# Kernel optimization log

Measured on AMD Instinct MI355X. Metric: run time of the kernel, lower is better.

Reference implementation:

```python
import jax, jax.numpy as jnp
import numpy as np

D_MODEL = 512
N_HEADS = 8
D_K = D_MODEL // N_HEADS  # 64
MAX_LEN = 5000


def _positional_encoding(d_model, max_len):
    pe = np.zeros((max_len, d_model), dtype=np.float32)
    position = np.arange(max_len, dtype=np.float32)[:, None]
    div_term = np.exp(np.arange(0, d_model, 2, dtype=np.float32) * (-np.log(10000.0) / d_model))
    pe[:, 0::2] = np.sin(position * div_term)
    pe[:, 1::2] = np.cos(position * div_term)
    return jnp.asarray(pe)


def _layer_norm(x, gamma, beta, eps):
    mu = jnp.mean(x, axis=-1, keepdims=True)
    var = jnp.mean(jnp.square(x - mu), axis=-1, keepdims=True)
    return (x - mu) * jax.lax.rsqrt(var + eps) * gamma + beta


def setup_inputs() -> dict:
    key = jax.random.key(0)
    ks = jax.random.split(key, 5)
    s = 1.0 / np.sqrt(D_MODEL)
    return {
        "x": jax.random.normal(ks[0], (4, 2048, D_MODEL), dtype=jnp.float32),
        "ln1_g": jnp.ones((D_MODEL,), jnp.float32),
        "ln1_b": jnp.zeros((D_MODEL,), jnp.float32),
        "wq": jax.random.normal(ks[1], (D_MODEL, D_MODEL), jnp.float32) * s,
        "wk": jax.random.normal(ks[2], (D_MODEL, D_MODEL), jnp.float32) * s,
        "wv": jax.random.normal(ks[3], (D_MODEL, D_MODEL), jnp.float32) * s,
        "wfc": jax.random.normal(ks[4], (D_MODEL, D_MODEL), jnp.float32) * s,
        "ln2_g": jnp.ones((D_MODEL,), jnp.float32),
        "ln2_b": jnp.zeros((D_MODEL,), jnp.float32),
    }


def reference(x, ln1_g, ln1_b, wq, wk, wv, wfc, ln2_g, ln2_b):
    B, T, D = x.shape
    residual0 = x
    # outer pre-norm (nn.LayerNorm default eps=1e-5)
    h = _layer_norm(x, ln1_g, ln1_b, 1e-5)
    # sinusoidal positional encoding
    h = h + _positional_encoding(D_MODEL, MAX_LEN)[:T]
    residual1 = h
    # projections -> [B, H, T, d]
    q = (h @ wq).reshape(B, T, N_HEADS, D_K).transpose(0, 2, 1, 3)
    k = (h @ wk).reshape(B, T, N_HEADS, D_K).transpose(0, 2, 1, 3)
    v = (h @ wv).reshape(B, T, N_HEADS, D_K).transpose(0, 2, 1, 3)
    scale = 1.0 / np.sqrt(D_K).astype(np.float32)
    attn = jnp.einsum("bhqd,bhkd->bhqk", q * scale, k)
    causal = jnp.tril(jnp.ones((T, T), dtype=bool))  # subsequent mask
    attn = jnp.where(causal, attn, jnp.float32(-1e9))
    attn = jax.nn.softmax(attn, axis=-1)
    o = jnp.einsum("bhqk,bhkd->bhqd", attn, v)
    o = o.transpose(0, 2, 1, 3).reshape(B, T, D)
    o = o @ wfc
    # inner post-attention residual + LayerNorm (eps=1e-6)
    h2 = _layer_norm(o + residual1, ln2_g, ln2_b, 1e-6)
    return h2 + residual0
```

## Files before the change

### kernel.cpp

```cpp
#include <hip/hip_runtime.h>
#include <hip/hip_bf16.h>

#define B_ 4
#define T_ 2048
#define D_ 512

typedef __attribute__((ext_vector_type(8))) short short8;
typedef __attribute__((ext_vector_type(4))) short short4v;
typedef __attribute__((ext_vector_type(4))) float float4v;
typedef unsigned short bf16_t;

__device__ __forceinline__ bf16_t f2bf(float f) {
  unsigned int u = __builtin_bit_cast(unsigned int, f);
  unsigned int r = (u + 0x7fffu + ((u >> 16) & 1u)) >> 16;
  return (bf16_t)r;
}
__device__ __forceinline__ float bf2f(bf16_t b) {
  unsigned int u = ((unsigned int)b) << 16;
  return __builtin_bit_cast(float, u);
}

__device__ __forceinline__ float waveReduceSum(float v) {
#pragma unroll
  for (int m = 32; m >= 1; m >>= 1) v += __shfl_xor(v, m, 64);
  return v;
}

__device__ __forceinline__ void gld16(const bf16_t* g, bf16_t* l) {
  __builtin_amdgcn_global_load_lds(
      (const __attribute__((address_space(1))) void*)g,
      (__attribute__((address_space(3))) void*)l, 16, 0, 0);
}

__global__ __launch_bounds__(256) void pre_kernel(
    const float* __restrict__ x, const float* __restrict__ g,
    const float* __restrict__ bb,
    const float* __restrict__ wq, const float* __restrict__ wk,
    const float* __restrict__ wv, const float* __restrict__ wfc,
    bf16_t* __restrict__ h_bf16,
    bf16_t* __restrict__ wqkvT, bf16_t* __restrict__ wfcT) {
  if (blockIdx.x >= 2048) {
    int bid = blockIdx.x - 2048;
#pragma unroll 4
    for (int i = 0; i < 16; ++i) {
      int idx = bid * 4096 + i * 256 + threadIdx.x;
      if (idx < 786432) {
        int n = idx >> 9, k = idx & 511;
        const float* src = (n < 512) ? wq : ((n < 1024) ? wk : wv);
        float scl = (n >= 512 && n < 1024) ? 0.125f : 1.0f;
        int c = n & 511;
        wqkvT[idx] = f2bf(src[k * 512 + c] * scl);
      } else {
        int j = idx - 786432;
        int n = j >> 9, k = j & 511;
        wfcT[j] = f2bf(wfc[k * 512 + n]);
      }
    }
    return;
  }
  int wave = threadIdx.x >> 6, lane = threadIdx.x & 63;
  int row = blockIdx.x * 4 + wave;
  int pos = row & (T_ - 1);
  const float* xr = x + (size_t)row * D_;
  int c0 = lane * 8;
  float v[8];
  float4 a = *(const float4*)(xr + c0);
  float4 b4 = *(const float4*)(xr + c0 + 4);
  v[0]=a.x; v[1]=a.y; v[2]=a.z; v[3]=a.w;
  v[4]=b4.x; v[5]=b4.y; v[6]=b4.z; v[7]=b4.w;
  float s = 0.f;
#pragma unroll
  for (int j = 0; j < 8; ++j) s += v[j];
  s = waveReduceSum(s);
  float mu = s * (1.f / 512.f);
  float q = 0.f;
#pragma unroll
  for (int j = 0; j < 8; ++j) { float d = v[j] - mu; q += d * d; }
  q = waveReduceSum(q);
  float rstd = rsqrtf(q * (1.f / 512.f) + 1e-5f);
  bf16_t* hb = h_bf16 + (size_t)row * D_;
#pragma unroll
  for (int j = 0; j < 8; ++j) {
    int col = c0 + j;
    float hn = (v[j] - mu) * rstd * g[col] + bb[col];
    int i2 = (col >> 1) << 1;
    float dt = __expf((float)i2 * (-9.2103403719761836f / 512.0f));
    float ang = (float)pos * dt;
    float pe = (col & 1) ? __cosf(ang) : __sinf(ang);
    hb[col] = f2bf(hn + pe);
  }
}

template <typename EPI>
__device__ __forceinline__ void gemm_body(const bf16_t* __restrict__ A,
                                          const bf16_t* __restrict__ Bt,
                                          int m0, int n0, bf16_t* As, bf16_t* Bs,
                                          EPI epi) {
  const int tid = threadIdx.x;
  const int w = tid >> 6, lane = tid & 63;
  const int ln = lane & 15, quad = lane >> 4;
  const int wy = w >> 1, wx = w & 1;
  const int sw = ln & 7;

  float4v acc[4][4];
  float4v z = {0.f, 0.f, 0.f, 0.f};
#pragma unroll
  for (int i = 0; i < 4; ++i)
#pragma unroll
    for (int j = 0; j < 4; ++j) acc[i][j] = z;

  for (int k0 = 0; k0 < 512; k0 += 64) {
#pragma unroll
    for (int i = 0; i < 4; ++i) {
      int cbase = w * 256 + i * 64;
      int chunk = cbase + lane;
      int row = chunk >> 3;
      int lb = (chunk & 7) ^ (row & 7);
      gld16(A + (size_t)(m0 + row) * 512 + k0 + lb * 8, As + cbase * 8);
      gld16(Bt + (size_t)(n0 + row) * 512 + k0 + lb * 8, Bs + cbase * 8);
    }
    __syncthreads();
#pragma unroll
    for (int c = 0; c < 2; ++c) {
      short8 af[4], bf[4];
#pragma unroll
      for (int mt = 0; mt < 4; ++mt)
        af[mt] = *(const short8*)(As + (wy * 64 + mt * 16 + ln) * 64 + (((c * 4 + quad) ^ sw)) * 8);
#pragma unroll
      for (int nt = 0; nt < 4; ++nt)
        bf[nt] = *(const short8*)(Bs + (wx * 64 + nt * 16 + ln) * 64 + (((c * 4 + quad) ^ sw)) * 8);
#pragma unroll
      for (int mt = 0; mt < 4; ++mt)
#pragma unroll
        for (int nt = 0; nt < 4; ++nt)
          acc[mt][nt] = __builtin_amdgcn_mfma_f32_16x16x32_bf16(af[mt], bf[nt], acc[mt][nt], 0, 0, 0);
    }
    __syncthreads();
  }
#pragma unroll
  for (int mt = 0; mt < 4; ++mt)
#pragma unroll
    for (int r = 0; r < 4; ++r) {
      int row = m0 + wy * 64 + mt * 16 + quad * 4 + r;
#pragma unroll
      for (int nt = 0; nt < 4; ++nt) {
        int col = n0 + wx * 64 + nt * 16 + ln;
        epi(row, col, acc[mt][nt][r]);
      }
    }
}

__global__ __launch_bounds__(256) void gemm_qkvt_kernel(
    const bf16_t* __restrict__ h_bf, const bf16_t* __restrict__ wqkvT,
    bf16_t* __restrict__ qk, bf16_t* __restrict__ vT) {
  __shared__ __align__(16) bf16_t As[128 * 64];
  __shared__ __align__(16) bf16_t Bs[128 * 64];
  int bx = blockIdx.x;
  if (bx < 512) {
    int m0 = (bx >> 3) * 128, n0 = (bx & 7) * 128;
    gemm_body(h_bf, wqkvT, m0, n0, As, Bs,
              [&](int row, int col, float v) { qk[(size_t)row * 1024 + col] = f2bf(v); });
  } else {
    int local = bx - 512;
    int m0 = (local >> 6) * 128, n0 = (local & 63) * 128;
    gemm_body(wqkvT + 1024 * 512, h_bf, m0, n0, As, Bs,
              [&](int row, int col, float v) { vT[(size_t)row * 8192 + col] = f2bf(v); });
  }
}

__global__ __launch_bounds__(256) void gemm_out_kernel(
    const bf16_t* __restrict__ attn, const bf16_t* __restrict__ wfcT,
    const bf16_t* __restrict__ h_bf, bf16_t* __restrict__ o2r) {
  __shared__ __align__(16) bf16_t As[128 * 64];
  __shared__ __align__(16) bf16_t Bs[128 * 64];
  int bx = blockIdx.x;
  int m0 = (bx >> 2) * 128, n0 = (bx & 3) * 128;
  gemm_body(attn, wfcT, m0, n0, As, Bs, [&](int row, int col, float v) {
    size_t o = (size_t)row * 512 + col;
    o2r[o] = f2bf(v + bf2f(h_bf[o]));
  });
}

__global__ __launch_bounds__(256) void attn_kernel(const bf16_t* __restrict__ qk,
                                                   const bf16_t* __restrict__ vT,
                                                   bf16_t* __restrict__ out) {
  __shared__ __align__(16) bf16_t Ks[2][64 * 64];
  __shared__ __align__(16) bf16_t Vs[2][64 * 64];
  const int bx = blockIdx.x;
  const int qt = 31 - (bx >> 5);
  const int bh = bx & 31;
  const int b = bh >> 3, h = bh & 7;
  const int tid = threadIdx.x;
  const int w = tid >> 6, lane = tid & 63;
  const int ln = lane & 15, quad = lane >> 4;
  const int sw = ln & 7;

  short8 qf0, qf1;
  {
    size_t qrow = ((size_t)b * T_ + qt * 64 + w * 16 + ln) * 1024 + h * 64;
    qf0 = *(const short8*)(qk + qrow + quad * 8);
    qf1 = *(const short8*)(qk + qrow + 32 + quad * 8);
  }
  float4v z = {0.f, 0.f, 0.f, 0.f};
  float4v oacc[4];
#pragma unroll
  for (int i = 0; i < 4; ++i) oacc[i] = z;
  float m_s = -1e30f, l_s = 0.f;

  const bf16_t* kbase = qk + (size_t)b * T_ * 1024 + 512 + h * 64;
  const bf16_t* vbase = vT + (size_t)(h * 64) * 8192 + (size_t)b * T_;

  auto stage = [&](int buf, int kt) {
#pragma unroll
    for (int i = 0; i < 2; ++i) {
      int cbase = w * 128 + i * 64;
      int chunk = cbase + lane;
      int row = chunk >> 3;
      int lb = (chunk & 7) ^ (row & 7);
      gld16(kbase + (size_t)(kt * 64 + row) * 1024 + lb * 8, Ks[buf] + (size_t)cbase * 8);
      gld16(vbase + (size_t)row * 8192 + kt * 64 + lb * 8, Vs[buf] + (size_t)cbase * 8);
    }
  };

  auto compute = [&](const bf16_t* Kc, const bf16_t* Vc, bool mask) {
    float sv[4][4];
#pragma unroll
    for (int mt = 0; mt < 4; ++mt) {
      float4v st = z;
      int row = mt * 16 + ln;
      short8 a0 = *(const short8*)(Kc + row * 64 + ((0 + quad) ^ sw) * 8);
      short8 a1 = *(const short8*)(Kc + row * 64 + ((4 + quad) ^ sw) * 8);
      st = __builtin_amdgcn_mfma_f32_16x16x32_bf16(a0, qf0, st, 0, 0, 0);
      st = __builtin_amdgcn_mfma_f32_16x16x32_bf16(a1, qf1, st, 0, 0, 0);
#pragma unroll
      for (int r = 0; r < 4; ++r) {
        float v = st[r];
        if (mask) {
          int kloc = mt * 16 + quad * 4 + r;
          if (kloc > w * 16 + ln) v = -1e30f;
        }
        sv[mt][r] = v;
      }
    }
    float mx = sv[0][0];
#pragma unroll
    for (int mt = 0; mt < 4; ++mt)
#pragma unroll
      for (int r = 0; r < 4; ++r) mx = fmaxf(mx, sv[mt][r]);
    mx = fmaxf(mx, __shfl_xor(mx, 16, 64));
    mx = fmaxf(mx, __shfl_xor(mx, 32, 64));
    float mn = fmaxf(m_s, mx);
    float alpha = __expf(m_s - mn);
    m_s = mn;
    float rs = 0.f;
#pragma unroll
    for (int mt = 0; mt < 4; ++mt)
#pragma unroll
      for (int r = 0; r < 4; ++r) {
        float p = __expf(sv[mt][r] - mn);
        sv[mt][r] = p;
        rs += p;
      }
    rs += __shfl_xor(rs, 16, 64);
    rs += __shfl_xor(rs, 32, 64);
    l_s = l_s * alpha + rs;
#pragma unroll
    for (int dt = 0; dt < 4; ++dt)
#pragma unroll
      for (int r = 0; r < 4; ++r) oacc[dt][r] *= alpha;
    short4v pf[4];
#pragma unroll
    for (int mt = 0; mt < 4; ++mt) {
      unsigned u0 = __builtin_bit_cast(unsigned, sv[mt][0]) + 0x8000u;
      unsigned u1 = __builtin_bit_cast(unsigned, sv[mt][1]) + 0x8000u;
      unsigned u2 = __builtin_bit_cast(unsigned, sv[mt][2]) + 0x8000u;
      unsigned u3 = __builtin_bit_cast(unsigned, sv[mt][3]) + 0x8000u;
      uint2 pp;
      pp.x = __builtin_amdgcn_perm(u1, u0, 0x07060302u);
      pp.y = __builtin_amdgcn_perm(u3, u2, 0x07060302u);
      pf[mt] = __builtin_bit_cast(short4v, pp);
    }
#pragma unroll
    for (int dt = 0; dt < 4; ++dt) {
      int row = dt * 16 + ln;
#pragma unroll
      for (int mt = 0; mt < 4; ++mt) {
        short4v av = *(const short4v*)(Vc + row * 64 + ((2 * mt + (quad >> 1)) ^ sw) * 8 + (quad & 1) * 4);
        oacc[dt] = __builtin_amdgcn_mfma_f32_16x16x16bf16_1k(av, pf[mt], oacc[dt], 0, 0, 0);
      }
    }
  };

  stage(0, 0);
  __syncthreads();
  for (int kt = 0; kt < qt; ++kt) {
    int cur = kt & 1;
    stage(cur ^ 1, kt + 1);
    compute(Ks[cur], Vs[cur], false);
    __syncthreads();
  }
  compute(Ks[qt & 1], Vs[qt & 1], true);

  float inv = 1.0f / l_s;
  size_t obase = ((size_t)b * T_ + qt * 64 + w * 16 + ln) * 512 + h * 64;
#pragma unroll
  for (int dt = 0; dt < 4; ++dt) {
    short4v o4;
#pragma unroll
    for (int r = 0; r < 4; ++r) o4[r] = (short)f2bf(oacc[dt][r] * inv);
    *(short4v*)(out + obase + dt * 16 + quad * 4) = o4;
  }
}

__global__ __launch_bounds__(256) void ln2_kernel(
    const bf16_t* __restrict__ o2r, const float* __restrict__ x,
    const float* __restrict__ g, const float* __restrict__ bb,
    float* __restrict__ out) {
  int wave = threadIdx.x >> 6, lane = threadIdx.x & 63;
  int row = blockIdx.x * 4 + wave;
  size_t ro = (size_t)row * D_;
  int c0 = lane * 8;
  short8 ov = *(const short8*)(o2r + ro + c0);
  float t[8];
#pragma unroll
  for (int j = 0; j < 8; ++j) t[j] = bf2f((bf16_t)ov[j]);
  float s = 0.f;
#pragma unroll
  for (int j = 0; j < 8; ++j) s += t[j];
  s = waveReduceSum(s);
  float mu = s * (1.f / 512.f);
  float q = 0.f;
#pragma unroll
  for (int j = 0; j < 8; ++j) { float d = t[j] - mu; q += d * d; }
  q = waveReduceSum(q);
  float rstd = rsqrtf(q * (1.f / 512.f) + 1e-6f);
  float4 x0 = *(const float4*)(x + ro + c0);
  float4 x1 = *(const float4*)(x + ro + c0 + 4);
  float xr[8] = {x0.x, x0.y, x0.z, x0.w, x1.x, x1.y, x1.z, x1.w};
  float o[8];
#pragma unroll
  for (int j = 0; j < 8; ++j) {
    int col = c0 + j;
    o[j] = (t[j] - mu) * rstd * g[col] + bb[col] + xr[j];
  }
  float4 w0 = {o[0], o[1], o[2], o[3]};
  float4 w1 = {o[4], o[5], o[6], o[7]};
  *(float4*)(out + ro + c0) = w0;
  *(float4*)(out + ro + c0 + 4) = w1;
}

extern "C" void kernel_launch(void* const* d_in, const int* in_sizes, int n_in,
                              void* d_out, int out_size, void* d_ws, size_t ws_size,
                              hipStream_t stream) {
  const float* x   = (const float*)d_in[0];
  const float* g1  = (const float*)d_in[1];
  const float* b1  = (const float*)d_in[2];
  const float* wq  = (const float*)d_in[3];
  const float* wk  = (const float*)d_in[4];
  const float* wv  = (const float*)d_in[5];
  const float* wfc = (const float*)d_in[6];
  const float* g2  = (const float*)d_in[7];
  const float* b2  = (const float*)d_in[8];
  float* out = (float*)d_out;

  char* ws = (char*)d_ws;
  const size_t O_HBF  = 0;
  const size_t O_WQKV = 8388608;
  const size_t O_WFC  = 9961472;
  const size_t O_QK   = 10485760;
  const size_t O_VT   = 27262976;
  const size_t O_ATTN = 35651584;
  const size_t O_O2R  = 44040192;
  const size_t WS_NEED = 52428800;
  if (ws_size < WS_NEED) return;

  bf16_t* h_bf  = (bf16_t*)(ws + O_HBF);
  bf16_t* wqkvT = (bf16_t*)(ws + O_WQKV);
  bf16_t* wfcT  = (bf16_t*)(ws + O_WFC);
  bf16_t* qk    = (bf16_t*)(ws + O_QK);
  bf16_t* vT    = (bf16_t*)(ws + O_VT);
  bf16_t* attn  = (bf16_t*)(ws + O_ATTN);
  bf16_t* o2r   = (bf16_t*)(ws + O_O2R);

  pre_kernel<<<dim3(2304), dim3(256), 0, stream>>>(x, g1, b1, wq, wk, wv, wfc,
                                                   h_bf, wqkvT, wfcT);
  gemm_qkvt_kernel<<<dim3(768), dim3(256), 0, stream>>>(h_bf, wqkvT, qk, vT);
  attn_kernel<<<dim3(1024), dim3(256), 0, stream>>>(qk, vT, attn);
  gemm_out_kernel<<<dim3(256), dim3(256), 0, stream>>>(attn, wfcT, h_bf, o2r);
  ln2_kernel<<<dim3(2048), dim3(256), 0, stream>>>(o2r, x, g2, b2, out);
}
```

Baseline: 185.2 us.

## Use exp2 softmax with folded log2e, lazy rescale, packed bf16 convert

```diff
diff --git a/kernel.cpp b/kernel.cpp
--- a/kernel.cpp
+++ b/kernel.cpp
@@ -18,6 +18,22 @@
 __device__ __forceinline__ float bf2f(bf16_t b) {
   unsigned int u = ((unsigned int)b) << 16;
   return __builtin_bit_cast(float, u);
+}
+
+__device__ __forceinline__ float fast_exp2(float x) {
+#if __has_builtin(__builtin_amdgcn_exp2f)
+  return __builtin_amdgcn_exp2f(x);
+#else
+  float r;
+  asm("v_exp_f32 %0, %1" : "=v"(r) : "v"(x));
+  return r;
+#endif
+}
+
+__device__ __forceinline__ unsigned cvt_pk_bf16(float lo, float hi) {
+  unsigned r;
+  asm("v_cvt_pk_bf16_f32 %0, %1, %2" : "=v"(r) : "v"(lo), "v"(hi));
+  return r;
 }
 
 __device__ __forceinline__ float waveReduceSum(float v) {
@@ -47,7 +63,8 @@
       if (idx < 786432) {
         int n = idx >> 9, k = idx & 511;
         const float* src = (n < 512) ? wq : ((n < 1024) ? wk : wv);
-        float scl = (n >= 512 && n < 1024) ? 0.125f : 1.0f;
+        float scl = (n < 512) ? 1.4426950408889634f
+                              : ((n < 1024) ? 0.125f : 1.0f);
         int c = n & 511;
         wqkvT[idx] = f2bf(src[k * 512 + c] * scl);
       } else {
@@ -79,15 +96,16 @@
   q = waveReduceSum(q);
   float rstd = rsqrtf(q * (1.f / 512.f) + 1e-5f);
   bf16_t* hb = h_bf16 + (size_t)row * D_;
-#pragma unroll
-  for (int j = 0; j < 8; ++j) {
-    int col = c0 + j;
-    float hn = (v[j] - mu) * rstd * g[col] + bb[col];
-    int i2 = (col >> 1) << 1;
-    float dt = __expf((float)i2 * (-9.2103403719761836f / 512.0f));
-    float ang = (float)pos * dt;
-    float pe = (col & 1) ? __cosf(ang) : __sinf(ang);
-    hb[col] = f2bf(hn + pe);
+  float fpos = (float)pos;
+#pragma unroll
+  for (int jp = 0; jp < 4; ++jp) {
+    int col = c0 + jp * 2;
+    float dt = fast_exp2((float)col * (-13.287712379549449f / 512.0f));
+    float ang = fpos * dt;
+    float hn0 = (v[2 * jp] - mu) * rstd * g[col] + bb[col] + __sinf(ang);
+    float hn1 = (v[2 * jp + 1] - mu) * rstd * g[col + 1] + bb[col + 1] + __cosf(ang);
+    hb[col] = f2bf(hn0);
+    hb[col + 1] = f2bf(hn1);
   }
 }
 
@@ -210,16 +228,22 @@
   const bf16_t* kbase = qk + (size_t)b * T_ * 1024 + 512 + h * 64;
   const bf16_t* vbase = vT + (size_t)(h * 64) * 8192 + (size_t)b * T_;
 
-  auto stage = [&](int buf, int kt) {
-#pragma unroll
-    for (int i = 0; i < 2; ++i) {
-      int cbase = w * 128 + i * 64;
-      int chunk = cbase + lane;
-      int row = chunk >> 3;
-      int lb = (chunk & 7) ^ (row & 7);
-      gld16(kbase + (size_t)(kt * 64 + row) * 1024 + lb * 8, Ks[buf] + (size_t)cbase * 8);
-      gld16(vbase + (size_t)row * 8192 + kt * 64 + lb * 8, Vs[buf] + (size_t)cbase * 8);
-    }
+  const int cb0 = w * 128, cb1 = w * 128 + 64;
+  const int ch0 = cb0 + lane, ch1 = cb1 + lane;
+  const int r0 = ch0 >> 3, r1 = ch1 >> 3;
+  const int lb0 = (ch0 & 7) ^ (r0 & 7), lb1 = (ch1 & 7) ^ (r1 & 7);
+  const bf16_t* kg0 = kbase + (size_t)r0 * 1024 + lb0 * 8;
+  const bf16_t* kg1 = kbase + (size_t)r1 * 1024 + lb1 * 8;
+  const bf16_t* vg0 = vbase + (size_t)r0 * 8192 + lb0 * 8;
+  const bf16_t* vg1 = vbase + (size_t)r1 * 8192 + lb1 * 8;
+
+  auto stage2 = [&](int buf) {
+    gld16(kg0, Ks[buf] + cb0 * 8);
+    gld16(kg1, Ks[buf] + cb1 * 8);
+    gld16(vg0, Vs[buf] + cb0 * 8);
+    gld16(vg1, Vs[buf] + cb1 * 8);
+    kg0 += 64 * 1024; kg1 += 64 * 1024;
+    vg0 += 64;        vg1 += 64;
   };
 
   auto compute = [&](const bf16_t* Kc, const bf16_t* Vc, bool mask) {
@@ -249,35 +273,34 @@
       for (int r = 0; r < 4; ++r) mx = fmaxf(mx, sv[mt][r]);
     mx = fmaxf(mx, __shfl_xor(mx, 16, 64));
     mx = fmaxf(mx, __shfl_xor(mx, 32, 64));
-    float mn = fmaxf(m_s, mx);
-    float alpha = __expf(m_s - mn);
-    m_s = mn;
+    if (!__all(mx <= m_s + 8.0f)) {
+      float mn = fmaxf(m_s, mx);
+      float alpha = fast_exp2(m_s - mn);
+      m_s = mn;
+      l_s *= alpha;
+#pragma unroll
+      for (int dt = 0; dt < 4; ++dt)
+#pragma unroll
+        for (int r = 0; r < 4; ++r) oacc[dt][r] *= alpha;
+    }
     float rs = 0.f;
 #pragma unroll
     for (int mt = 0; mt < 4; ++mt)
 #pragma unroll
       for (int r = 0; r < 4; ++r) {
-        float p = __expf(sv[mt][r] - mn);
+        float p = fast_exp2(sv[mt][r] - m_s);
         sv[mt][r] = p;
         rs += p;
       }
     rs += __shfl_xor(rs, 16, 64);
     rs += __shfl_xor(rs, 32, 64);
-    l_s = l_s * alpha + rs;
-#pragma unroll
-    for (int dt = 0; dt < 4; ++dt)
-#pragma unroll
-      for (int r = 0; r < 4; ++r) oacc[dt][r] *= alpha;
+    l_s += rs;
     short4v pf[4];
 #pragma unroll
     for (int mt = 0; mt < 4; ++mt) {
-      unsigned u0 = __builtin_bit_cast(unsigned, sv[mt][0]) + 0x8000u;
-      unsigned u1 = __builtin_bit_cast(unsigned, sv[mt][1]) + 0x8000u;
-      unsigned u2 = __builtin_bit_cast(unsigned, sv[mt][2]) + 0x8000u;
-      unsigned u3 = __builtin_bit_cast(unsigned, sv[mt][3]) + 0x8000u;
       uint2 pp;
-      pp.x = __builtin_amdgcn_perm(u1, u0, 0x07060302u);
-      pp.y = __builtin_amdgcn_perm(u3, u2, 0x07060302u);
+      pp.x = cvt_pk_bf16(sv[mt][0], sv[mt][1]);
+      pp.y = cvt_pk_bf16(sv[mt][2], sv[mt][3]);
       pf[mt] = __builtin_bit_cast(short4v, pp);
     }
 #pragma unroll
@@ -291,11 +314,11 @@
     }
   };
 
-  stage(0, 0);
+  stage2(0);
   __syncthreads();
   for (int kt = 0; kt < qt; ++kt) {
     int cur = kt & 1;
-    stage(cur ^ 1, kt + 1);
+    stage2(cur ^ 1);
     compute(Ks[cur], Vs[cur], false);
     __syncthreads();
   }
```

After: 180.7 us. -2.4%, faster.
